# Performance work log

Measured on AMD Instinct MI355X. Metric: run time of the kernel, lower is better.

## Reference

```python
import jax, jax.numpy as jnp
import numpy as np
import math

B, L, D, NUM_TYPES = 4, 4096, 512, 22
T_MAX = 200.0
SIGMA, LAMBD = 10.0, 0.005


def setup_inputs() -> dict:
    key = jax.random.key(0)
    k1, k2, k3 = jax.random.split(key, 3)
    event_type = jax.random.randint(k1, (B, L), 0, NUM_TYPES + 1)
    # event times in [0, t_max), sorted along the sequence (realistic point process)
    event_time = jnp.sort(jax.random.uniform(k2, (B, L), dtype=jnp.float32) * T_MAX, axis=-1)
    # embedding table with padding row 0 zeroed (padding_idx=0)
    emb_table = jax.random.normal(k3, (NUM_TYPES + 1, D), dtype=jnp.float32).at[0].set(0.0)
    return {"event_type": event_type, "event_time": event_time, "emb_table": emb_table}


def reference(event_type, event_time, emb_table):
    d_model = emb_table.shape[1]
    seq_len = event_time.shape[1]

    # sinusoidal temporal encoding: t / 10000^(2*(i//2)/d)
    i = jnp.arange(d_model)
    pos_vec = jnp.power(jnp.float32(10000.0), 2.0 * (i // 2).astype(jnp.float32) / d_model)
    temp = event_time[:, :, None] / pos_vec  # [B, L, D]
    temp_enc = jnp.where(i % 2 == 0, jnp.sin(temp), jnp.cos(temp))

    type_embedding = emb_table[event_type] * math.sqrt(d_model)  # [B, L, D]
    embedding = jnp.concatenate([temp_enc, type_embedding], axis=-1)  # [B, L, 2D]

    # RBF kernel pairwise scores: sigma^2 * exp(-(|ti - tj|^norm)^2 / lambd^2), norm=2
    t = event_time / T_MAX  # normalized times
    d = jnp.abs(t[:, :, None] - t[:, None, :]) ** 2  # [B, L, L]
    scores = (SIGMA ** 2) * jnp.exp(-(d ** 2) / (LAMBD ** 2))

    # causal mask: keep j <= i, fill future with -1000, then softmax over rows
    causal = jnp.tril(jnp.ones((seq_len, seq_len), dtype=bool))  # [L, L]
    scores = jnp.where(causal[None, :, :], scores, jnp.float32(-1000.0))
    scores = jax.nn.softmax(scores, axis=-1)
    return scores, embedding
```

## Files before the change

kernel.cpp:

```cpp
#include <hip/hip_runtime.h>

#define SEQ_L 4096
#define BATCH 4
#define DMODEL 512
#define STRIPE 512
#define RPW 4
#define RPB 16
#define SCORE_BLOCKS (BATCH * SEQ_L / RPB)
#define EMB_BLOCKS 512
#define NBLK (SCORE_BLOCKS + EMB_BLOCKS)

typedef float f4 __attribute__((ext_vector_type(4)));

__global__ __launch_bounds__(256) void fused_kernel(const int* __restrict__ et,
                                                    const float* __restrict__ tm,
                                                    const float* __restrict__ tab,
                                                    float* __restrict__ scores,
                                                    float* __restrict__ emb) {
    const int bid = blockIdx.x;

    if (bid % 3 != 2) {
        const int sidx = bid - bid / 3;
        const int b  = sidx >> 8;
        const int i0 = (sidx & 255) * RPB;
        const int wave = threadIdx.x >> 6;
        const int lane = threadIdx.x & 63;
        const int ibase = i0 + wave * RPW;

        const float* tb  = tm + b * SEQ_L;
        const f4*    tb4 = (const f4*)tb;
        const float inv200 = 1.0f / 200.0f;

        int LSc[RPW], RSc[RPW];
        #pragma unroll
        for (int r = 0; r < RPW; ++r) {
            const int i = ibase + r;
            int ls = i - STRIPE; if (ls < 0) ls = 0;
            ls &= ~31;
            const int rs = (i & ~31) + 32;
            LSc[r] = ls >> 2; RSc[r] = rs >> 2;
        }

        const f4 z = {0.f, 0.f, 0.f, 0.f};
        #pragma unroll
        for (int r = 0; r < RPW; ++r) {
            f4* out4 = (f4*)(scores + ((size_t)(b * SEQ_L + ibase + r)) * SEQ_L);
            for (int c = RSc[r] + lane; c < SEQ_L / 4; c += 64) out4[c] = z;
        }
        #pragma unroll
        for (int r = 0; r < RPW; ++r) {
            f4* out4 = (f4*)(scores + ((size_t)(b * SEQ_L + ibase + r)) * SEQ_L);
            for (int c = lane; c < LSc[r]; c += 64) out4[c] = z;
        }

        float tiR[RPW], invR[RPW];
        #pragma unroll
        for (int r = 0; r < RPW; ++r) {
            const int i = ibase + r;
            const float ti = tb[i] * inv200;
            tiR[r] = ti;
            float sum = 0.0f;
            for (int j = 4 * LSc[r] + lane; j <= i; j += 64) {
                float d = ti - tb[j] * inv200;
                float d2 = d * d;
                float s = 100.0f * __expf(-(d2 * d2) * 40000.0f);
                sum += __expf(s - 100.0f);
            }
            #pragma unroll
            for (int off = 1; off < 64; off <<= 1) sum += __shfl_xor(sum, off, 64);
            invR[r] = 1.0f / sum;
        }

        #pragma unroll
        for (int r = 0; r < RPW; ++r) {
            const int i = ibase + r;
            const float ti = tiR[r], inv = invR[r];
            f4* out4 = (f4*)(scores + ((size_t)(b * SEQ_L + i)) * SEQ_L);
            for (int c = LSc[r] + lane; c < RSc[r]; c += 64) {
                f4 tv = tb4[c];
                f4 v;
                #pragma unroll
                for (int q = 0; q < 4; ++q) {
                    const int jj = 4 * c + q;
                    float d = ti - tv[q] * inv200;
                    float d2 = d * d;
                    float s = 100.0f * __expf(-(d2 * d2) * 40000.0f);
                    float p = __expf(s - 100.0f) * inv;
                    v[q] = (jj <= i) ? p : 0.0f;
                }
                out4[c] = v;
            }
        }
    } else {
        const int t = threadIdx.x;
        const bool temporal = t < 128;

        float ipA = 0.0f, ipB = 0.0f;
        if (temporal) {
            const float c = -13.287712379549449f / 256.0f;
            ipA = exp2f(c * (float)(2 * t));
            ipB = exp2f(c * (float)(2 * t + 1));
        }
        const int ecol = (t - 128) * 4;

        const int eidx = bid / 3;
        const int bl0 = eidx * 32;
        for (int r = 0; r < 32; ++r) {
            const int bl = bl0 + r;
            f4 v;
            if (temporal) {
                const float time = tm[bl];
                const float a = time * ipA;
                const float bp = time * ipB;
                v[0] = __sinf(a);  v[1] = __cosf(a);
                v[2] = __sinf(bp); v[3] = __cosf(bp);
            } else {
                f4 e = *(const f4*)(tab + et[bl] * DMODEL + ecol);
                v = e * 22.627416997969522f;
            }
            ((f4*)(emb + (size_t)bl * 2 * DMODEL))[t] = v;
        }
    }
}

extern "C" void kernel_launch(void* const* d_in, const int* in_sizes, int n_in,
                              void* d_out, int out_size, void* d_ws, size_t ws_size,
                              hipStream_t stream) {
    const int*   event_type = (const int*)d_in[0];
    const float* event_time = (const float*)d_in[1];
    const float* emb_table  = (const float*)d_in[2];

    float* scores = (float*)d_out;
    float* emb    = scores + (size_t)BATCH * SEQ_L * SEQ_L;

    fused_kernel<<<NBLK, 256, 0, stream>>>(
        event_type, event_time, emb_table, scores, emb);
}
```

Measured before the change: 71.25 us.

## Split row-sum pass into param kernel and flatten output into persistent linear sweep

Moves the per-row softmax normalizer computation into a separate small kernel that writes (t_i, 1/sum) pairs to workspace. The main kernel then becomes a persistent grid-stride sweep where each wave writes one contiguous 1KB chunk of the combined scores+embedding output, computing the banded values only where needed. The aim is perfectly linear, evenly spread store traffic across the huge output instead of per-row blocks with imbalanced zero-fill. It adds a second launch, a workspace round trip, and per-chunk branching.

```diff
diff --git a/kernel.cpp b/kernel.cpp
--- a/kernel.cpp
+++ b/kernel.cpp
@@ -4,122 +4,97 @@
 #define BATCH 4
 #define DMODEL 512
 #define STRIPE 512
-#define RPW 4
-#define RPB 16
-#define SCORE_BLOCKS (BATCH * SEQ_L / RPB)
-#define EMB_BLOCKS 512
-#define NBLK (SCORE_BLOCKS + EMB_BLOCKS)
 
 typedef float f4 __attribute__((ext_vector_type(4)));
 
-__global__ __launch_bounds__(256) void fused_kernel(const int* __restrict__ et,
+#define SCG  (BATCH * SEQ_L * (SEQ_L / 4) / 64)
+#define EMBG (BATCH * SEQ_L * (2 * DMODEL / 4) / 64)
+#define TOTG (SCG + EMBG)
+#define BBLK 2048
+#define WB   (BBLK * 4)
+
+__global__ __launch_bounds__(256) void param_kernel(const float* __restrict__ tm,
+                                                    float2* __restrict__ ws) {
+    const int lane = threadIdx.x & 63;
+    const int gw = blockIdx.x * 4 + (threadIdx.x >> 6);
+    const float inv200 = 1.0f / 200.0f;
+    for (int r = 0; r < 16; ++r) {
+        const int row = gw * 16 + r;
+        const int b = row >> 12, i = row & (SEQ_L - 1);
+        const float* tb = tm + b * SEQ_L;
+        const float ti = tb[i] * inv200;
+        int ls = i - STRIPE; if (ls < 0) ls = 0;
+        ls &= ~31;
+        float sum = 0.0f;
+        for (int j = ls + lane; j <= i; j += 64) {
+            float d = ti - tb[j] * inv200;
+            float d2 = d * d;
+            float s = 100.0f * __expf(-(d2 * d2) * 40000.0f);
+            sum += __expf(s - 100.0f);
+        }
+        #pragma unroll
+        for (int off = 1; off < 64; off <<= 1) sum += __shfl_xor(sum, off, 64);
+        if (lane == 0) ws[row] = make_float2(ti, 1.0f / sum);
+    }
+}
+
+__global__ __launch_bounds__(256) void sweep_kernel(const int* __restrict__ et,
                                                     const float* __restrict__ tm,
                                                     const float* __restrict__ tab,
-                                                    float* __restrict__ scores,
-                                                    float* __restrict__ emb) {
-    const int bid = blockIdx.x;
+                                                    const float2* __restrict__ ws,
+                                                    float* __restrict__ out) {
+    const int lane = threadIdx.x & 63;
+    const int w = blockIdx.x * 4 + (threadIdx.x >> 6);
+    f4* base = (f4*)out;
+    const f4 z = {0.f, 0.f, 0.f, 0.f};
+    const float inv200 = 1.0f / 200.0f;
 
-    if (bid % 3 != 2) {
-        const int sidx = bid - bid / 3;
-        const int b  = sidx >> 8;
-        const int i0 = (sidx & 255) * RPB;
-        const int wave = threadIdx.x >> 6;
-        const int lane = threadIdx.x & 63;
-        const int ibase = i0 + wave * RPW;
-
-        const float* tb  = tm + b * SEQ_L;
-        const f4*    tb4 = (const f4*)tb;
-        const float inv200 = 1.0f / 200.0f;
-
-        int LSc[RPW], RSc[RPW];
-        #pragma unroll
-        for (int r = 0; r < RPW; ++r) {
-            const int i = ibase + r;
+    for (int G = w; G < TOTG; G += WB) {
+        f4 v = z;
+        if (G < SCG) {
+            const int row = G >> 4;
+            const int c0 = (G & 15) << 6;
+            const int i = row & (SEQ_L - 1);
+            const int b = row >> 12;
             int ls = i - STRIPE; if (ls < 0) ls = 0;
             ls &= ~31;
-            const int rs = (i & ~31) + 32;
-            LSc[r] = ls >> 2; RSc[r] = rs >> 2;
-        }
-
-        const f4 z = {0.f, 0.f, 0.f, 0.f};
-        #pragma unroll
-        for (int r = 0; r < RPW; ++r) {
-            f4* out4 = (f4*)(scores + ((size_t)(b * SEQ_L + ibase + r)) * SEQ_L);
-            for (int c = RSc[r] + lane; c < SEQ_L / 4; c += 64) out4[c] = z;
-        }
-        #pragma unroll
-        for (int r = 0; r < RPW; ++r) {
-            f4* out4 = (f4*)(scores + ((size_t)(b * SEQ_L + ibase + r)) * SEQ_L);
-            for (int c = lane; c < LSc[r]; c += 64) out4[c] = z;
-        }
-
-        float tiR[RPW], invR[RPW];
-        #pragma unroll
-        for (int r = 0; r < RPW; ++r) {
-            const int i = ibase + r;
-            const float ti = tb[i] * inv200;
-            tiR[r] = ti;
-            float sum = 0.0f;
-            for (int j = 4 * LSc[r] + lane; j <= i; j += 64) {
-                float d = ti - tb[j] * inv200;
-                float d2 = d * d;
-                float s = 100.0f * __expf(-(d2 * d2) * 40000.0f);
-                sum += __expf(s - 100.0f);
+            const int ls4 = ls >> 2;
+            const int rs4 = ((i & ~31) + 32) >> 2;
+            if (c0 + 64 > ls4 && c0 < rs4) {
+                const int c = c0 + lane;
+                if (c >= ls4 && c < rs4) {
+                    const float2 pr = ws[row];
+                    const f4 tv = ((const f4*)(tm + b * SEQ_L))[c];
+                    #pragma unroll
+                    for (int q = 0; q < 4; ++q) {
+                        const int jj = 4 * c + q;
+                        float d = pr.x - tv[q] * inv200;
+                        float d2 = d * d;
+                        float s = 100.0f * __expf(-(d2 * d2) * 40000.0f);
+                        float p = __expf(s - 100.0f) * pr.y;
+                        v[q] = (jj <= i) ? p : 0.0f;
+                    }
+                }
             }
-            #pragma unroll
-            for (int off = 1; off < 64; off <<= 1) sum += __shfl_xor(sum, off, 64);
-            invR[r] = 1.0f / sum;
-        }
-
-        #pragma unroll
-        for (int r = 0; r < RPW; ++r) {
-            const int i = ibase + r;
-            const float ti = tiR[r], inv = invR[r];
-            f4* out4 = (f4*)(scores + ((size_t)(b * SEQ_L + i)) * SEQ_L);
-            for (int c = LSc[r] + lane; c < RSc[r]; c += 64) {
-                f4 tv = tb4[c];
-                f4 v;
-                #pragma unroll
-                for (int q = 0; q < 4; ++q) {
-                    const int jj = 4 * c + q;
-                    float d = ti - tv[q] * inv200;
-                    float d2 = d * d;
-                    float s = 100.0f * __expf(-(d2 * d2) * 40000.0f);
-                    float p = __expf(s - 100.0f) * inv;
-                    v[q] = (jj <= i) ? p : 0.0f;
-                }
-                out4[c] = v;
-            }
-        }
-    } else {
-        const int t = threadIdx.x;
-        const bool temporal = t < 128;
-
-        float ipA = 0.0f, ipB = 0.0f;
-        if (temporal) {
-            const float c = -13.287712379549449f / 256.0f;
-            ipA = exp2f(c * (float)(2 * t));
-            ipB = exp2f(c * (float)(2 * t + 1));
-        }
-        const int ecol = (t - 128) * 4;
-
-        const int eidx = bid / 3;
-        const int bl0 = eidx * 32;
-        for (int r = 0; r < 32; ++r) {
-            const int bl = bl0 + r;
-            f4 v;
-            if (temporal) {
-                const float time = tm[bl];
-                const float a = time * ipA;
-                const float bp = time * ipB;
+        } else {
+            const int eg = G - SCG;
+            const int row = eg >> 2;
+            const int c = ((eg & 3) << 6) + lane;
+            if (c < 128) {
+                const float time = tm[row];
+                const float C2 = -13.287712379549449f / 512.0f;
+                const int k0 = 4 * c;
+                const float ipA = exp2f(C2 * (float)k0);
+                const float ipB = exp2f(C2 * (float)(k0 + 2));
+                const float a = time * ipA, bp = time * ipB;
                 v[0] = __sinf(a);  v[1] = __cosf(a);
                 v[2] = __sinf(bp); v[3] = __cosf(bp);
             } else {
-                f4 e = *(const f4*)(tab + et[bl] * DMODEL + ecol);
+                const f4 e = *(const f4*)(tab + et[row] * DMODEL + (4 * c - DMODEL));
                 v = e * 22.627416997969522f;
             }
-            ((f4*)(emb + (size_t)bl * 2 * DMODEL))[t] = v;
         }
+        base[(size_t)G * 64 + lane] = v;
     }
 }
 
@@ -130,9 +105,7 @@
     const float* event_time = (const float*)d_in[1];
     const float* emb_table  = (const float*)d_in[2];
 
-    float* scores = (float*)d_out;
-    float* emb    = scores + (size_t)BATCH * SEQ_L * SEQ_L;
-
-    fused_kernel<<<NBLK, 256, 0, stream>>>(
-        event_type, event_time, emb_table, scores, emb);
+    param_kernel<<<256, 256, 0, stream>>>(event_time, (float2*)d_ws);
+    sweep_kernel<<<BBLK, 256, 0, stream>>>(event_type, event_time, emb_table,
+                                           (const float2*)d_ws, (float*)d_out);
 }
```

After: 92.34 us. 29.6% more time.
